# Kernel tuning notes

Measured on AMD Instinct MI355X. Metric: run time of the kernel, lower is better.

## Reference

```python
import jax, jax.numpy as jnp
import numpy as np

N = 100000
E = 1600000
IN_DIM, HID_DIM, OUT_DIM = 128, 64, 64


def setup_inputs() -> dict:
    key = jax.random.key(0)
    ks = jax.random.split(key, 8)
    x = jax.random.normal(ks[0], (N, IN_DIM), dtype=jnp.float32)
    src = jax.random.randint(ks[1], (E,), 0, N, dtype=jnp.int32)
    dst = jax.random.randint(ks[2], (E,), 0, N, dtype=jnp.int32)
    edge_index = jnp.stack([src, dst], axis=0)
    edge_weight = jax.random.uniform(ks[3], (E,), dtype=jnp.float32)
    # GCNConv params: lin weight [out, in] (no bias in lin), separate bias [out]
    W1 = jax.random.normal(ks[4], (HID_DIM, IN_DIM), dtype=jnp.float32) / np.sqrt(IN_DIM)
    b1 = jnp.zeros((HID_DIM,), dtype=jnp.float32)
    W2 = jax.random.normal(ks[5], (OUT_DIM, HID_DIM), dtype=jnp.float32) / np.sqrt(HID_DIM)
    b2 = jnp.zeros((OUT_DIM,), dtype=jnp.float32)
    return {"x": x, "edge_index": edge_index, "edge_weight": edge_weight,
            "W1": W1, "b1": b1, "W2": W2, "b2": b2}


def _gcn_conv(x, src, dst, ew, W, b, n_nodes):
    # PyG GCNConv: add self-loops (weight 1), symmetric normalization,
    # linear transform, scatter-add aggregation at dst, then bias.
    loop = jnp.arange(n_nodes, dtype=src.dtype)
    src_full = jnp.concatenate([src, loop])          # [E+N]
    dst_full = jnp.concatenate([dst, loop])          # [E+N]
    ew_full = jnp.concatenate([ew, jnp.ones((n_nodes,), x.dtype)])
    deg = jax.ops.segment_sum(ew_full, dst_full, num_segments=n_nodes)
    dinv = jnp.where(deg > 0, jax.lax.rsqrt(deg), 0.0)  # deg^{-1/2}, inf -> 0
    norm = dinv[src_full] * ew_full * dinv[dst_full]    # [E+N]
    h = x @ W.T                                          # [N, out]
    msgs = h[src_full] * norm[:, None]                   # gather + scale
    out = jax.ops.segment_sum(msgs, dst_full, num_segments=n_nodes)
    return out + b


def reference(x, edge_index, edge_weight, W1, b1, W2, b2):
    src, dst = edge_index[0], edge_index[1]
    h = _gcn_conv(x, src, dst, edge_weight, W1, b1, N)
    h = jax.nn.relu(h)
    # dropout is identity in eval mode (training=False)
    out = _gcn_conv(h, src, dst, edge_weight, W2, b2, N)
    return out
```

## Files before the change

kernel.cpp:

```cpp
#include <hip/hip_runtime.h>
#include <hip/hip_fp16.h>


constexpr float FXS     = 1048576.0f;
constexpr float FXS_INV = 1.0f / 1048576.0f;
constexpr int   SH      = 8;
constexpr int   CAP     = 5120;
constexpr int   NBMAX   = 512;
constexpr int   PW      = 256;
constexpr int   RPW     = 264;
constexpr int   BINA_BLOCKS = 256;

__device__ void binA_body(int bid, int nblocks,
                          const int* __restrict__ src, const int* __restrict__ dst,
                          const float* __restrict__ ew,
                          int* __restrict__ bktcur, int2* __restrict__ stage,
                          int E, int N) {
    __shared__ int cnt[NBMAX], gbase[NBMAX];
    const int tid = threadIdx.x;
    const int tot = E + N;
    const int nchunks = (tot + 2047) >> 11;
    for (int c = bid; c < nchunks; c += nblocks) {
        const int base = c << 11;
        for (int i = tid; i < NBMAX; i += 256) cnt[i] = 0;
        __syncthreads();
        int bkt[8], rank[8], pck[8];
        float w[8];
        #pragma unroll
        for (int j = 0; j < 8; ++j) {
            int e = base + j * 256 + tid;
            bkt[j] = -1;
            if (e < tot) {
                int s, t; float wv;
                if (e < E) { t = dst[e]; s = src[e]; wv = ew[e]; }
                else       { t = e - E;  s = t;      wv = 1.0f; }
                bkt[j] = t >> SH;
                pck[j] = ((t & 255) << 17) | s;
                w[j] = wv;
                rank[j] = atomicAdd(&cnt[bkt[j]], 1);
            }
        }
        __syncthreads();
        for (int i = tid; i < NBMAX; i += 256)
            if (cnt[i] > 0) gbase[i] = atomicAdd(&bktcur[i], cnt[i]);
        __syncthreads();
        #pragma unroll
        for (int j = 0; j < 8; ++j)
            if (bkt[j] >= 0) {
                int p = gbase[bkt[j]] + rank[j];
                if (p < CAP)
                    stage[(size_t)bkt[j] * CAP + p] =
                        make_int2(pck[j], __float_as_int(w[j]));
            }
        __syncthreads();
    }
}

template <int K, bool RELU>
__device__ void gemm_body(int bid, const float* __restrict__ X,
                          const float* __restrict__ W,
                          __half* __restrict__ H, int n) {
    constexpr int BK = 64, BK4 = 16;
    constexpr int XP = 68, WP = 68;
    __shared__ float Xs[64 * XP];
    __shared__ float Ws[BK * WP];
    const int tid = threadIdx.x;
    const int bn0 = bid * 64;
    const int tx = tid & 15, ty = tid >> 4;
    const int f0 = 4 * tx, nl = 4 * ty;

    float acc[4][4] = {};

    for (int kb = 0; kb < K; kb += BK) {
        #pragma unroll
        for (int it = 0; it < 4; ++it) {
            int idx = tid + it * 256;
            int node = idx >> 4, k4 = idx & 15;
            int g = bn0 + node;
            float4 v = make_float4(0.f, 0.f, 0.f, 0.f);
            if (g < n)
                v = *reinterpret_cast<const float4*>(X + (size_t)g * K + kb + 4 * k4);
            if (RELU) {
                v.x = fmaxf(v.x, 0.f); v.y = fmaxf(v.y, 0.f);
                v.z = fmaxf(v.z, 0.f); v.w = fmaxf(v.w, 0.f);
            }
            *reinterpret_cast<float4*>(&Xs[node * XP + 4 * k4]) = v;
        }
        #pragma unroll
        for (int it = 0; it < 4; ++it) {
            int idx = tid + it * 256;
            int feat = idx >> 4, k4 = idx & 15;
            float4 v = *reinterpret_cast<const float4*>(W + feat * K + kb + 4 * k4);
            Ws[(4 * k4 + 0) * WP + feat] = v.x;
            Ws[(4 * k4 + 1) * WP + feat] = v.y;
            Ws[(4 * k4 + 2) * WP + feat] = v.z;
            Ws[(4 * k4 + 3) * WP + feat] = v.w;
        }
        __syncthreads();

        #pragma unroll 4
        for (int k4 = 0; k4 < BK4; ++k4) {
            float4 xv[4], wv[4];
            #pragma unroll
            for (int i = 0; i < 4; ++i)
                xv[i] = *reinterpret_cast<const float4*>(&Xs[(nl + i) * XP + 4 * k4]);
            #pragma unroll
            for (int c = 0; c < 4; ++c)
                wv[c] = *reinterpret_cast<const float4*>(&Ws[(4 * k4 + c) * WP + f0]);
            #pragma unroll
            for (int i = 0; i < 4; ++i) {
                const float xc[4] = {xv[i].x, xv[i].y, xv[i].z, xv[i].w};
                #pragma unroll
                for (int c = 0; c < 4; ++c) {
                    acc[i][0] = fmaf(xc[c], wv[c].x, acc[i][0]);
                    acc[i][1] = fmaf(xc[c], wv[c].y, acc[i][1]);
                    acc[i][2] = fmaf(xc[c], wv[c].z, acc[i][2]);
                    acc[i][3] = fmaf(xc[c], wv[c].w, acc[i][3]);
                }
            }
        }
        __syncthreads();
    }

    #pragma unroll
    for (int i = 0; i < 4; ++i) {
        int g = bn0 + nl + i;
        if (g < n) {
            union { __half h[4]; uint2 u; } cv;
            cv.h[0] = __float2half_rn(acc[i][0]);
            cv.h[1] = __float2half_rn(acc[i][1]);
            cv.h[2] = __float2half_rn(acc[i][2]);
            cv.h[3] = __float2half_rn(acc[i][3]);
            *reinterpret_cast<uint2*>(H + ((size_t)g << 6) + f0) = cv.u;
        }
    }
}

__global__ __launch_bounds__(256, 4) void k_fat(const int* __restrict__ ei,
                                                const float* __restrict__ ew,
                                                int* __restrict__ bktcur,
                                                int2* __restrict__ stage,
                                                const float* __restrict__ x,
                                                const float* __restrict__ W1,
                                                __half* __restrict__ h16,
                                                int E, int N) {
    if (blockIdx.x < BINA_BLOCKS)
        binA_body(blockIdx.x, BINA_BLOCKS, ei, ei + E, ew, bktcur, stage, E, N);
    else
        gemm_body<128, false>(blockIdx.x - BINA_BLOCKS, x, W1, h16, N);
}

__global__ __launch_bounds__(256, 4) void k_gemm2(const float* __restrict__ X,
                                                  const float* __restrict__ W,
                                                  __half* __restrict__ H, int n) {
    gemm_body<64, true>(blockIdx.x, X, W, H, n);
}

__global__ __launch_bounds__(256) void k_histsort(
    const int2* __restrict__ stage, const int* __restrict__ bsizes,
    float* __restrict__ dinv, int* __restrict__ rowptr,
    int* __restrict__ winstart, int2* __restrict__ edata,
    const float* __restrict__ b1, const float* __restrict__ b2,
    float* __restrict__ agg1, float* __restrict__ dout,
    int N, int NB, int Etot) {
    __shared__ int2 eb[CAP];
    __shared__ unsigned long long hh[256];
    __shared__ int psum[256];
    __shared__ int cur[256];
    __shared__ float df[256];
    const int tid = threadIdx.x, b = blockIdx.x;

    int part = 0;
    for (int i = tid; i < b; i += 256) part += min(bsizes[i], CAP);
    psum[tid] = part;
    __syncthreads();
    for (int off = 128; off > 0; off >>= 1) {
        if (tid < off) psum[tid] += psum[tid + off];
        __syncthreads();
    }
    const int base = psum[0];
    const int len = min(bsizes[b], CAP);
    __syncthreads();

    hh[tid] = 0ull;
    __syncthreads();
    for (int i = tid; i < len; i += 256) {
        int2 en = stage[(size_t)b * CAP + i];
        eb[i] = en;
        unsigned long long fx = __float2uint_rn(__int_as_float(en.y) * FXS);
        atomicAdd(&hh[((unsigned)en.x) >> 17], (1ull << 32) | fx);
    }
    __syncthreads();

    const int c = (int)(hh[tid] >> 32);
    psum[tid] = c;
    __syncthreads();
    for (int off = 1; off < 256; off <<= 1) {
        int xv = (tid >= off) ? psum[tid - off] : 0;
        __syncthreads();
        psum[tid] += xv;
        __syncthreads();
    }
    const int rs = base + psum[tid] - c;
    const int g = (b << SH) + tid;
    float dv = 0.f;
    if (g < N) {
        dv = rsqrtf((float)(hh[tid] & 0xffffffffull) * FXS_INV);
        dinv[g] = dv;
        rowptr[g] = rs;
        const int re = rs + c;
        for (int w = (rs + PW - 1) / PW; w * PW < re; ++w) winstart[w] = g;
        if ((rs / PW) != ((re - 1) / PW)) {
            const float4* pb1 = (const float4*)b1;
            const float4* pb2 = (const float4*)b2;
            float4* pa = (float4*)(agg1 + ((size_t)g << 6));
            float4* po = (float4*)(dout + ((size_t)g << 6));
            #pragma unroll
            for (int j = 0; j < 16; ++j) { pa[j] = pb1[j]; po[j] = pb2[j]; }
        }
    }
    cur[tid] = rs;
    df[tid] = dv;
    if (b == 0 && tid == 0) rowptr[N] = Etot;
    __syncthreads();

    for (int i = tid; i < len; i += 256) {
        int2 en = eb[i];
        int local = ((unsigned)en.x) >> 17;
        int s = en.x & 0x1FFFF;
        float wsc = __int_as_float(en.y) * df[local];
        int pos = atomicAdd(&cur[local], 1);
        edata[pos] = make_int2(s, __float_as_int(wsc));
    }
}

__global__ __launch_bounds__(256) void k_pull(const int* __restrict__ rowptr,
                                              const int* __restrict__ winstart,
                                              const int2* __restrict__ edata,
                                              const __half* __restrict__ H,
                                              const float* __restrict__ dinv,
                                              const float* __restrict__ bias,
                                              float* __restrict__ AGG,
                                              int nW, int Etot, int N) {
    __shared__ int2 eb[4][PW];
    __shared__ int rp[4][RPW];
    const int wv = threadIdx.x >> 6, lane = threadIdx.x & 63;
    const int gq = lane >> 4;
    const int f4 = (lane & 15) * 4;
    const float4 bs = *reinterpret_cast<const float4*>(bias + f4);
    const int wid = blockIdx.x * 4 + wv;
    if (wid >= nW) return;
    const int e0 = wid * PW;
    const int e1 = min(e0 + PW, Etot);
    #pragma unroll
    for (int j = 0; j < PW / 64; ++j) {
        int e = e0 + j * 64 + lane;
        if (e < Etot) eb[wv][j * 64 + lane] = edata[e];
    }
    const int n0 = winstart[wid];
    #pragma unroll
    for (int j = 0; j < (RPW + 63) / 64; ++j) {
        int idx = j * 64 + lane;
        if (idx < RPW) {
            int nn = n0 + idx;
            rp[wv][idx] = (nn <= N) ? rowptr[nn] : Etot;
        }
    }
    int n = n0, e = e0;
    int rs = rp[wv][0];
    while (e < e1) {
        const int ni = n - n0 + 1;
        const int re = (ni < RPW) ? rp[wv][ni] : rowptr[n + 1];
        const int seg_end = min(re, e1);
        if (seg_end > e) {
            float a0 = 0.f, a1 = 0.f, a2 = 0.f, a3 = 0.f;
            int i = e - e0;
            const int iend = seg_end - e0;
            for (; i + 16 <= iend; i += 16) {
                int2 ed[4];
                uint2 hv[4];
                float ds[4];
                #pragma unroll
                for (int j = 0; j < 4; ++j) ed[j] = eb[wv][i + 4 * j + gq];
                #pragma unroll
                for (int j = 0; j < 4; ++j)
                    hv[j] = *reinterpret_cast<const uint2*>(
                        H + (((size_t)ed[j].x) << 6) + f4);
                #pragma unroll
                for (int j = 0; j < 4; ++j) ds[j] = dinv[ed[j].x];
                #pragma unroll
                for (int j = 0; j < 4; ++j) {
                    const float nr = ds[j] * __int_as_float(ed[j].y);
                    const __half2* ph = reinterpret_cast<const __half2*>(&hv[j]);
                    float2 p01 = __half22float2(ph[0]);
                    float2 p23 = __half22float2(ph[1]);
                    a0 = fmaf(p01.x, nr, a0);
                    a1 = fmaf(p01.y, nr, a1);
                    a2 = fmaf(p23.x, nr, a2);
                    a3 = fmaf(p23.y, nr, a3);
                }
            }
            for (; i < iend; i += 4) {
                int idx = i + gq;
                int2 ed = eb[wv][min(idx, iend - 1)];
                float nr = (idx < iend)
                               ? dinv[ed.x] * __int_as_float(ed.y) : 0.f;
                uint2 hv = *reinterpret_cast<const uint2*>(
                    H + (((size_t)ed.x) << 6) + f4);
                const __half2* ph = reinterpret_cast<const __half2*>(&hv);
                float2 p01 = __half22float2(ph[0]);
                float2 p23 = __half22float2(ph[1]);
                a0 = fmaf(p01.x, nr, a0);
                a1 = fmaf(p01.y, nr, a1);
                a2 = fmaf(p23.x, nr, a2);
                a3 = fmaf(p23.y, nr, a3);
            }
            a0 += __shfl_xor(a0, 16); a0 += __shfl_xor(a0, 32);
            a1 += __shfl_xor(a1, 16); a1 += __shfl_xor(a1, 32);
            a2 += __shfl_xor(a2, 16); a2 += __shfl_xor(a2, 32);
            a3 += __shfl_xor(a3, 16); a3 += __shfl_xor(a3, 32);
            if (lane < 16) {
                float* p = AGG + ((size_t)n << 6) + f4;
                if (rs >= e0 && re <= e1) {
                    *reinterpret_cast<float4*>(p) =
                        make_float4(a0 + bs.x, a1 + bs.y, a2 + bs.z, a3 + bs.w);
                } else {
                    atomicAdd(p + 0, a0);
                    atomicAdd(p + 1, a1);
                    atomicAdd(p + 2, a2);
                    atomicAdd(p + 3, a3);
                }
            }
        }
        e = seg_end;
        rs = re;
        ++n;
    }
}

extern "C" void kernel_launch(void* const* d_in, const int* in_sizes, int n_in,
                              void* d_out, int out_size, void* d_ws, size_t ws_size,
                              hipStream_t stream) {
    const float* x  = (const float*)d_in[0];
    const int*   ei = (const int*)d_in[1];
    const float* ew = (const float*)d_in[2];
    const float* W1 = (const float*)d_in[3];
    const float* b1 = (const float*)d_in[4];
    const float* W2 = (const float*)d_in[5];
    const float* b2 = (const float*)d_in[6];

    const int N = in_sizes[0] / 128;
    const int E = in_sizes[2];
    const int Etot = E + N;
    const int NB = (N + 255) >> SH;
    const int nW = (Etot + PW - 1) / PW;

    float* ws = (float*)d_ws;
    size_t o = 0;
    float*  dinv     = ws + o;            o += N;
    int*    rowptr   = (int*)(ws + o);    o += (size_t)N + 1;
    int*    winstart = (int*)(ws + o);    o += nW;
    int*    bktcur   = (int*)(ws + o);    o += NBMAX;
    o = (o + 1) & ~(size_t)1;
    int2*   edata    = (int2*)(ws + o);   o += 2 * (size_t)Etot;
    int2*   stage    = (int2*)(ws + o);   o += 2 * (size_t)NB * CAP;
    __half* h16      = (__half*)(ws + o); o += 32 * (size_t)N;
    float*  agg1     = ws + o;            o += 64 * (size_t)N;
    float*  out      = (float*)d_out;

    dim3 blk(256);
    const int gemm_blocks = (N + 63) / 64;

    hipMemsetAsync(bktcur, 0, NBMAX * sizeof(int), stream);
    k_fat<<<BINA_BLOCKS + gemm_blocks, blk, 0, stream>>>(ei, ew, bktcur, stage,
                                                         x, W1, h16, E, N);
    k_histsort<<<NB, blk, 0, stream>>>(stage, bktcur, dinv, rowptr, winstart,
                                       edata, b1, b2, agg1, out, N, NB, Etot);

    const int pull_blocks = (nW + 3) / 4;
    k_pull<<<pull_blocks, blk, 0, stream>>>(rowptr, winstart, edata, h16, dinv,
                                            b1, agg1, nW, Etot, N);
    k_gemm2<<<gemm_blocks, blk, 0, stream>>>(agg1, W2, h16, N);
    k_pull<<<pull_blocks, blk, 0, stream>>>(rowptr, winstart, edata, h16, dinv,
                                            b2, out, nW, Etot, N);
}
```

Before: 235.4 us.

## Split feature matrix into 16-column quarter planes and pull per quarter

```diff
diff --git a/kernel.cpp b/kernel.cpp
--- a/kernel.cpp
+++ b/kernel.cpp
@@ -59,7 +59,7 @@
 template <int K, bool RELU>
 __device__ void gemm_body(int bid, const float* __restrict__ X,
                           const float* __restrict__ W,
-                          __half* __restrict__ H, int n) {
+                          __half* __restrict__ Hq, int n) {
     constexpr int BK = 64, BK4 = 16;
     constexpr int XP = 68, WP = 68;
     __shared__ float Xs[64 * XP];
@@ -122,6 +122,7 @@
         __syncthreads();
     }
 
+    const int q = f0 >> 4, r = f0 & 15;
     #pragma unroll
     for (int i = 0; i < 4; ++i) {
         int g = bn0 + nl + i;
@@ -131,7 +132,7 @@
             cv.h[1] = __float2half_rn(acc[i][1]);
             cv.h[2] = __float2half_rn(acc[i][2]);
             cv.h[3] = __float2half_rn(acc[i][3]);
-            *reinterpret_cast<uint2*>(H + ((size_t)g << 6) + f0) = cv.u;
+            *reinterpret_cast<uint2*>(Hq + ((size_t)q * n + g) * 16 + r) = cv.u;
         }
     }
 }
@@ -142,32 +143,29 @@
                                                 int2* __restrict__ stage,
                                                 const float* __restrict__ x,
                                                 const float* __restrict__ W1,
-                                                __half* __restrict__ h16,
+                                                __half* __restrict__ Hq,
                                                 int E, int N) {
     if (blockIdx.x < BINA_BLOCKS)
         binA_body(blockIdx.x, BINA_BLOCKS, ei, ei + E, ew, bktcur, stage, E, N);
     else
-        gemm_body<128, false>(blockIdx.x - BINA_BLOCKS, x, W1, h16, N);
+        gemm_body<128, false>(blockIdx.x - BINA_BLOCKS, x, W1, Hq, N);
 }
 
 __global__ __launch_bounds__(256, 4) void k_gemm2(const float* __restrict__ X,
                                                   const float* __restrict__ W,
-                                                  __half* __restrict__ H, int n) {
-    gemm_body<64, true>(blockIdx.x, X, W, H, n);
-}
-
-__global__ __launch_bounds__(256) void k_histsort(
+                                                  __half* __restrict__ Hq, int n) {
+    gemm_body<64, true>(blockIdx.x, X, W, Hq, n);
+}
+
+__global__ __launch_bounds__(256) void k_hist(
     const int2* __restrict__ stage, const int* __restrict__ bsizes,
     float* __restrict__ dinv, int* __restrict__ rowptr,
-    int* __restrict__ winstart, int2* __restrict__ edata,
+    int* __restrict__ winstart,
     const float* __restrict__ b1, const float* __restrict__ b2,
     float* __restrict__ agg1, float* __restrict__ dout,
-    int N, int NB, int Etot) {
-    __shared__ int2 eb[CAP];
+    int N, int Etot) {
     __shared__ unsigned long long hh[256];
     __shared__ int psum[256];
-    __shared__ int cur[256];
-    __shared__ float df[256];
     const int tid = threadIdx.x, b = blockIdx.x;
 
     int part = 0;
@@ -186,7 +184,6 @@
     __syncthreads();
     for (int i = tid; i < len; i += 256) {
         int2 en = stage[(size_t)b * CAP + i];
-        eb[i] = en;
         unsigned long long fx = __float2uint_rn(__int_as_float(en.y) * FXS);
         atomicAdd(&hh[((unsigned)en.x) >> 17], (1ull << 32) | fx);
     }
@@ -203,10 +200,8 @@
     }
     const int rs = base + psum[tid] - c;
     const int g = (b << SH) + tid;
-    float dv = 0.f;
     if (g < N) {
-        dv = rsqrtf((float)(hh[tid] & 0xffffffffull) * FXS_INV);
-        dinv[g] = dv;
+        dinv[g] = rsqrtf((float)(hh[tid] & 0xffffffffull) * FXS_INV);
         rowptr[g] = rs;
         const int re = rs + c;
         for (int w = (rs + PW - 1) / PW; w * PW < re; ++w) winstart[w] = g;
@@ -219,37 +214,51 @@
             for (int j = 0; j < 16; ++j) { pa[j] = pb1[j]; po[j] = pb2[j]; }
         }
     }
-    cur[tid] = rs;
-    df[tid] = dv;
     if (b == 0 && tid == 0) rowptr[N] = Etot;
-    __syncthreads();
-
+}
+
+__global__ __launch_bounds__(256) void k_sort(const int2* __restrict__ stage,
+                                              const int* __restrict__ bsizes,
+                                              const int* __restrict__ rowptr,
+                                              const float* __restrict__ dinv,
+                                              int2* __restrict__ edata, int N) {
+    __shared__ int cur[256];
+    __shared__ float df[256];
+    const int tid = threadIdx.x, b = blockIdx.x;
+    const int g = (b << SH) + tid;
+    if (g < N) {
+        cur[tid] = rowptr[g];
+        df[tid] = dinv[g];
+    }
+    __syncthreads();
+    const int len = min(bsizes[b], CAP);
     for (int i = tid; i < len; i += 256) {
-        int2 en = eb[i];
+        int2 en = stage[(size_t)b * CAP + i];
         int local = ((unsigned)en.x) >> 17;
         int s = en.x & 0x1FFFF;
-        float wsc = __int_as_float(en.y) * df[local];
+        float nr = dinv[s] * __int_as_float(en.y) * df[local];
         int pos = atomicAdd(&cur[local], 1);
-        edata[pos] = make_int2(s, __float_as_int(wsc));
-    }
-}
-
-__global__ __launch_bounds__(256) void k_pull(const int* __restrict__ rowptr,
-                                              const int* __restrict__ winstart,
-                                              const int2* __restrict__ edata,
-                                              const __half* __restrict__ H,
-                                              const float* __restrict__ dinv,
-                                              const float* __restrict__ bias,
-                                              float* __restrict__ AGG,
-                                              int nW, int Etot, int N) {
+        edata[pos] = make_int2(s, __float_as_int(nr));
+    }
+}
+
+__global__ __launch_bounds__(256) void k_pullq(const int* __restrict__ rowptr,
+                                               const int* __restrict__ winstart,
+                                               const int2* __restrict__ edata,
+                                               const __half* __restrict__ Hq,
+                                               const float* __restrict__ bias,
+                                               float* __restrict__ AGG,
+                                               int nW, int Etot, int N, int BPP) {
     __shared__ int2 eb[4][PW];
     __shared__ int rp[4][RPW];
     const int wv = threadIdx.x >> 6, lane = threadIdx.x & 63;
     const int gq = lane >> 4;
-    const int f4 = (lane & 15) * 4;
-    const float4 bs = *reinterpret_cast<const float4*>(bias + f4);
-    const int wid = blockIdx.x * 4 + wv;
+    const int f  = lane & 15;
+    const int qPass = blockIdx.x / BPP;
+    const int wid = (blockIdx.x - qPass * BPP) * 4 + wv;
     if (wid >= nW) return;
+    const __half* HB = Hq + (size_t)qPass * N * 16;
+    const float bf = bias[(qPass << 4) + f];
     const int e0 = wid * PW;
     const int e1 = min(e0 + PW, Etot);
     #pragma unroll
@@ -273,63 +282,33 @@
         const int re = (ni < RPW) ? rp[wv][ni] : rowptr[n + 1];
         const int seg_end = min(re, e1);
         if (seg_end > e) {
-            float a0 = 0.f, a1 = 0.f, a2 = 0.f, a3 = 0.f;
+            float a = 0.f;
             int i = e - e0;
             const int iend = seg_end - e0;
             for (; i + 16 <= iend; i += 16) {
                 int2 ed[4];
-                uint2 hv[4];
-                float ds[4];
+                __half hv[4];
                 #pragma unroll
                 for (int j = 0; j < 4; ++j) ed[j] = eb[wv][i + 4 * j + gq];
                 #pragma unroll
                 for (int j = 0; j < 4; ++j)
-                    hv[j] = *reinterpret_cast<const uint2*>(
-                        H + (((size_t)ed[j].x) << 6) + f4);
+                    hv[j] = HB[(size_t)ed[j].x * 16 + f];
                 #pragma unroll
-                for (int j = 0; j < 4; ++j) ds[j] = dinv[ed[j].x];
-                #pragma unroll
-                for (int j = 0; j < 4; ++j) {
-                    const float nr = ds[j] * __int_as_float(ed[j].y);
-                    const __half2* ph = reinterpret_cast<const __half2*>(&hv[j]);
-                    float2 p01 = __half22float2(ph[0]);
-                    float2 p23 = __half22float2(ph[1]);
-                    a0 = fmaf(p01.x, nr, a0);
-                    a1 = fmaf(p01.y, nr, a1);
-                    a2 = fmaf(p23.x, nr, a2);
-                    a3 = fmaf(p23.y, nr, a3);
-                }
+                for (int j = 0; j < 4; ++j)
+                    a = fmaf(__half2float(hv[j]), __int_as_float(ed[j].y), a);
             }
             for (; i < iend; i += 4) {
                 int idx = i + gq;
                 int2 ed = eb[wv][min(idx, iend - 1)];
-                float nr = (idx < iend)
-                               ? dinv[ed.x] * __int_as_float(ed.y) : 0.f;
-                uint2 hv = *reinterpret_cast<const uint2*>(
-                    H + (((size_t)ed.x) << 6) + f4);
-                const __half2* ph = reinterpret_cast<const __half2*>(&hv);
-                float2 p01 = __half22float2(ph[0]);
-                float2 p23 = __half22float2(ph[1]);
-                a0 = fmaf(p01.x, nr, a0);
-                a1 = fmaf(p01.y, nr, a1);
-                a2 = fmaf(p23.x, nr, a2);
-                a3 = fmaf(p23.y, nr, a3);
-            }
-            a0 += __shfl_xor(a0, 16); a0 += __shfl_xor(a0, 32);
-            a1 += __shfl_xor(a1, 16); a1 += __shfl_xor(a1, 32);
-            a2 += __shfl_xor(a2, 16); a2 += __shfl_xor(a2, 32);
-            a3 += __shfl_xor(a3, 16); a3 += __shfl_xor(a3, 32);
+                float nr = (idx < iend) ? __int_as_float(ed.y) : 0.f;
+                a = fmaf(__half2float(HB[(size_t)ed.x * 16 + f]), nr, a);
+            }
+            a += __shfl_xor(a, 16);
+            a += __shfl_xor(a, 32);
             if (lane < 16) {
-                float* p = AGG + ((size_t)n << 6) + f4;
-                if (rs >= e0 && re <= e1) {
-                    *reinterpret_cast<float4*>(p) =
-                        make_float4(a0 + bs.x, a1 + bs.y, a2 + bs.z, a3 + bs.w);
-                } else {
-                    atomicAdd(p + 0, a0);
-                    atomicAdd(p + 1, a1);
-                    atomicAdd(p + 2, a2);
-                    atomicAdd(p + 3, a3);
-                }
+                float* p = AGG + ((size_t)n << 6) + (qPass << 4) + lane;
+                if (rs >= e0 && re <= e1) *p = a + bf;
+                else atomicAdd(p, a);
             }
         }
         e = seg_end;
@@ -354,6 +333,7 @@
     const int Etot = E + N;
     const int NB = (N + 255) >> SH;
     const int nW = (Etot + PW - 1) / PW;
+    const int BPP = (nW + 3) / 4;
 
     float* ws = (float*)d_ws;
     size_t o = 0;
@@ -364,7 +344,7 @@
     o = (o + 1) & ~(size_t)1;
     int2*   edata    = (int2*)(ws + o);   o += 2 * (size_t)Etot;
     int2*   stage    = (int2*)(ws + o);   o += 2 * (size_t)NB * CAP;
-    __half* h16      = (__half*)(ws + o); o += 32 * (size_t)N;
+    __half* Hq       = (__half*)(ws + o); o += 32 * (size_t)N;
     float*  agg1     = ws + o;            o += 64 * (size_t)N;
     float*  out      = (float*)d_out;
 
@@ -373,14 +353,14 @@
 
     hipMemsetAsync(bktcur, 0, NBMAX * sizeof(int), stream);
     k_fat<<<BINA_BLOCKS + gemm_blocks, blk, 0, stream>>>(ei, ew, bktcur, stage,
-                                                         x, W1, h16, E, N);
-    k_histsort<<<NB, blk, 0, stream>>>(stage, bktcur, dinv, rowptr, winstart,
-                                       edata, b1, b2, agg1, out, N, NB, Etot);
-
-    const int pull_blocks = (nW + 3) / 4;
-    k_pull<<<pull_blocks, blk, 0, stream>>>(rowptr, winstart, edata, h16, dinv,
-                                            b1, agg1, nW, Etot, N);
-    k_gemm2<<<gemm_blocks, blk, 0, stream>>>(agg1, W2, h16, N);
-    k_pull<<<pull_blocks, blk, 0, stream>>>(rowptr, winstart, edata, h16, dinv,
-                                            b2, out, nW, Etot, N);
-}
+                                                         x, W1, Hq, E, N);
+    k_hist<<<NB, blk, 0, stream>>>(stage, bktcur, dinv, rowptr, winstart,
+                                   b1, b2, agg1, out, N, Etot);
+    k_sort<<<NB, blk, 0, stream>>>(stage, bktcur, rowptr, dinv, edata, N);
+
+    k_pullq<<<4 * BPP, blk, 0, stream>>>(rowptr, winstart, edata, Hq, b1, agg1,
+                                         nW, Etot, N, BPP);
+    k_gemm2<<<gemm_blocks, blk, 0, stream>>>(agg1, W2, Hq, N);
+    k_pullq<<<4 * BPP, blk, 0, stream>>>(rowptr, winstart, edata, Hq, b2, out,
+                                         nW, Etot, N, BPP);
+}
```

Measured after the change: 326.7 us. +38.8%, slower.

## Handle self-loops analytically and fold full edge normalization into sorted edge data

Applied to the files above, without the earlier changes.

```diff
diff --git a/kernel.cpp b/kernel.cpp
--- a/kernel.cpp
+++ b/kernel.cpp
@@ -15,11 +15,10 @@
                           const int* __restrict__ src, const int* __restrict__ dst,
                           const float* __restrict__ ew,
                           int* __restrict__ bktcur, int2* __restrict__ stage,
-                          int E, int N) {
+                          int E) {
     __shared__ int cnt[NBMAX], gbase[NBMAX];
     const int tid = threadIdx.x;
-    const int tot = E + N;
-    const int nchunks = (tot + 2047) >> 11;
+    const int nchunks = (E + 2047) >> 11;
     for (int c = bid; c < nchunks; c += nblocks) {
         const int base = c << 11;
         for (int i = tid; i < NBMAX; i += 256) cnt[i] = 0;
@@ -30,13 +29,11 @@
         for (int j = 0; j < 8; ++j) {
             int e = base + j * 256 + tid;
             bkt[j] = -1;
-            if (e < tot) {
-                int s, t; float wv;
-                if (e < E) { t = dst[e]; s = src[e]; wv = ew[e]; }
-                else       { t = e - E;  s = t;      wv = 1.0f; }
+            if (e < E) {
+                int t = dst[e];
                 bkt[j] = t >> SH;
-                pck[j] = ((t & 255) << 17) | s;
-                w[j] = wv;
+                pck[j] = ((t & 255) << 17) | src[e];
+                w[j] = ew[e];
                 rank[j] = atomicAdd(&cnt[bkt[j]], 1);
             }
         }
@@ -56,10 +53,14 @@
     }
 }
 
-template <int K, bool RELU>
+template <int K, bool RELU, bool BINIT>
 __device__ void gemm_body(int bid, const float* __restrict__ X,
                           const float* __restrict__ W,
-                          __half* __restrict__ H, int n) {
+                          __half* __restrict__ H, int n,
+                          const char* __restrict__ flags,
+                          const float* __restrict__ dinv,
+                          const float* __restrict__ bias,
+                          float* __restrict__ OUT) {
     constexpr int BK = 64, BK4 = 16;
     constexpr int XP = 68, WP = 68;
     __shared__ float Xs[64 * XP];
@@ -132,6 +133,18 @@
             cv.h[2] = __float2half_rn(acc[i][2]);
             cv.h[3] = __float2half_rn(acc[i][3]);
             *reinterpret_cast<uint2*>(H + ((size_t)g << 6) + f0) = cv.u;
+            if (BINIT) {
+                if (flags[g]) {
+                    const float d = dinv[g];
+                    const float d2 = d * d;
+                    const float4 bs = *reinterpret_cast<const float4*>(bias + f0);
+                    *reinterpret_cast<float4*>(OUT + ((size_t)g << 6) + f0) =
+                        make_float4(fmaf(acc[i][0], d2, bs.x),
+                                    fmaf(acc[i][1], d2, bs.y),
+                                    fmaf(acc[i][2], d2, bs.z),
+                                    fmaf(acc[i][3], d2, bs.w));
+                }
+            }
         }
     }
 }
@@ -145,29 +158,30 @@
                                                 __half* __restrict__ h16,
                                                 int E, int N) {
     if (blockIdx.x < BINA_BLOCKS)
-        binA_body(blockIdx.x, BINA_BLOCKS, ei, ei + E, ew, bktcur, stage, E, N);
+        binA_body(blockIdx.x, BINA_BLOCKS, ei, ei + E, ew, bktcur, stage, E);
     else
-        gemm_body<128, false>(blockIdx.x - BINA_BLOCKS, x, W1, h16, N);
+        gemm_body<128, false, false>(blockIdx.x - BINA_BLOCKS, x, W1, h16, N,
+                                     nullptr, nullptr, nullptr, nullptr);
 }
 
 __global__ __launch_bounds__(256, 4) void k_gemm2(const float* __restrict__ X,
                                                   const float* __restrict__ W,
-                                                  __half* __restrict__ H, int n) {
-    gemm_body<64, true>(blockIdx.x, X, W, H, n);
-}
-
-__global__ __launch_bounds__(256) void k_histsort(
+                                                  __half* __restrict__ H, int n,
+                                                  const char* __restrict__ flags,
+                                                  const float* __restrict__ dinv,
+                                                  const float* __restrict__ bias,
+                                                  float* __restrict__ OUT) {
+    gemm_body<64, true, true>(blockIdx.x, X, W, H, n, flags, dinv, bias, OUT);
+}
+
+__global__ __launch_bounds__(256) void k_hist(
     const int2* __restrict__ stage, const int* __restrict__ bsizes,
     float* __restrict__ dinv, int* __restrict__ rowptr,
-    int* __restrict__ winstart, int2* __restrict__ edata,
-    const float* __restrict__ b1, const float* __restrict__ b2,
-    float* __restrict__ agg1, float* __restrict__ dout,
-    int N, int NB, int Etot) {
-    __shared__ int2 eb[CAP];
+    int* __restrict__ winstart, char* __restrict__ flags,
+    const __half* __restrict__ h16, const float* __restrict__ b1,
+    float* __restrict__ agg1, int N, int E) {
     __shared__ unsigned long long hh[256];
     __shared__ int psum[256];
-    __shared__ int cur[256];
-    __shared__ float df[256];
     const int tid = threadIdx.x, b = blockIdx.x;
 
     int part = 0;
@@ -186,7 +200,6 @@
     __syncthreads();
     for (int i = tid; i < len; i += 256) {
         int2 en = stage[(size_t)b * CAP + i];
-        eb[i] = en;
         unsigned long long fx = __float2uint_rn(__int_as_float(en.y) * FXS);
         atomicAdd(&hh[((unsigned)en.x) >> 17], (1ull << 32) | fx);
     }
@@ -203,34 +216,55 @@
     }
     const int rs = base + psum[tid] - c;
     const int g = (b << SH) + tid;
-    float dv = 0.f;
     if (g < N) {
-        dv = rsqrtf((float)(hh[tid] & 0xffffffffull) * FXS_INV);
+        const float dv =
+            rsqrtf(1.0f + (float)(hh[tid] & 0xffffffffull) * FXS_INV);
         dinv[g] = dv;
         rowptr[g] = rs;
         const int re = rs + c;
         for (int w = (rs + PW - 1) / PW; w * PW < re; ++w) winstart[w] = g;
-        if ((rs / PW) != ((re - 1) / PW)) {
-            const float4* pb1 = (const float4*)b1;
-            const float4* pb2 = (const float4*)b2;
+        const bool flagged = (c == 0) || ((rs / PW) != ((re - 1) / PW));
+        flags[g] = flagged ? 1 : 0;
+        if (flagged) {
+            const float d2 = dv * dv;
+            const __half2* hp = (const __half2*)(h16 + ((size_t)g << 6));
+            const float4* pb = (const float4*)b1;
             float4* pa = (float4*)(agg1 + ((size_t)g << 6));
-            float4* po = (float4*)(dout + ((size_t)g << 6));
             #pragma unroll
-            for (int j = 0; j < 16; ++j) { pa[j] = pb1[j]; po[j] = pb2[j]; }
-        }
-    }
-    cur[tid] = rs;
-    df[tid] = dv;
-    if (b == 0 && tid == 0) rowptr[N] = Etot;
-    __syncthreads();
-
+            for (int j = 0; j < 16; ++j) {
+                float2 fA = __half22float2(hp[2 * j]);
+                float2 fB = __half22float2(hp[2 * j + 1]);
+                float4 bb = pb[j];
+                pa[j] = make_float4(fmaf(fA.x, d2, bb.x), fmaf(fA.y, d2, bb.y),
+                                    fmaf(fB.x, d2, bb.z), fmaf(fB.y, d2, bb.w));
+            }
+        }
+    }
+    if (b == 0 && tid == 0) rowptr[N] = E;
+}
+
+__global__ __launch_bounds__(256) void k_sort(const int2* __restrict__ stage,
+                                              const int* __restrict__ bsizes,
+                                              const int* __restrict__ rowptr,
+                                              const float* __restrict__ dinv,
+                                              int2* __restrict__ edata, int N) {
+    __shared__ int cur[256];
+    __shared__ float df[256];
+    const int tid = threadIdx.x, b = blockIdx.x;
+    const int g = (b << SH) + tid;
+    if (g < N) {
+        cur[tid] = rowptr[g];
+        df[tid] = dinv[g];
+    }
+    __syncthreads();
+    const int len = min(bsizes[b], CAP);
     for (int i = tid; i < len; i += 256) {
-        int2 en = eb[i];
+        int2 en = stage[(size_t)b * CAP + i];
         int local = ((unsigned)en.x) >> 17;
         int s = en.x & 0x1FFFF;
-        float wsc = __int_as_float(en.y) * df[local];
+        float nr = dinv[s] * __int_as_float(en.y) * df[local];
         int pos = atomicAdd(&cur[local], 1);
-        edata[pos] = make_int2(s, __float_as_int(wsc));
+        edata[pos] = make_int2(s, __float_as_int(nr));
     }
 }
 
@@ -241,7 +275,7 @@
                                               const float* __restrict__ dinv,
                                               const float* __restrict__ bias,
                                               float* __restrict__ AGG,
-                                              int nW, int Etot, int N) {
+                                              int nW, int E, int N) {
     __shared__ int2 eb[4][PW];
     __shared__ int rp[4][RPW];
     const int wv = threadIdx.x >> 6, lane = threadIdx.x & 63;
@@ -251,11 +285,11 @@
     const int wid = blockIdx.x * 4 + wv;
     if (wid >= nW) return;
     const int e0 = wid * PW;
-    const int e1 = min(e0 + PW, Etot);
+    const int e1 = min(e0 + PW, E);
     #pragma unroll
     for (int j = 0; j < PW / 64; ++j) {
         int e = e0 + j * 64 + lane;
-        if (e < Etot) eb[wv][j * 64 + lane] = edata[e];
+        if (e < E) eb[wv][j * 64 + lane] = edata[e];
     }
     const int n0 = winstart[wid];
     #pragma unroll
@@ -263,23 +297,24 @@
         int idx = j * 64 + lane;
         if (idx < RPW) {
             int nn = n0 + idx;
-            rp[wv][idx] = (nn <= N) ? rowptr[nn] : Etot;
+            rp[wv][idx] = (nn <= N) ? rowptr[nn] : E;
         }
     }
     int n = n0, e = e0;
     int rs = rp[wv][0];
     while (e < e1) {
-        const int ni = n - n0 + 1;
-        const int re = (ni < RPW) ? rp[wv][ni] : rowptr[n + 1];
+        const int re = rp[wv][n - n0 + 1];
         const int seg_end = min(re, e1);
         if (seg_end > e) {
+            const uint2 hs = *reinterpret_cast<const uint2*>(
+                H + ((size_t)n << 6) + f4);
+            const float dv = dinv[n];
             float a0 = 0.f, a1 = 0.f, a2 = 0.f, a3 = 0.f;
             int i = e - e0;
             const int iend = seg_end - e0;
             for (; i + 16 <= iend; i += 16) {
                 int2 ed[4];
                 uint2 hv[4];
-                float ds[4];
                 #pragma unroll
                 for (int j = 0; j < 4; ++j) ed[j] = eb[wv][i + 4 * j + gq];
                 #pragma unroll
@@ -287,10 +322,8 @@
                     hv[j] = *reinterpret_cast<const uint2*>(
                         H + (((size_t)ed[j].x) << 6) + f4);
                 #pragma unroll
-                for (int j = 0; j < 4; ++j) ds[j] = dinv[ed[j].x];
-                #pragma unroll
                 for (int j = 0; j < 4; ++j) {
-                    const float nr = ds[j] * __int_as_float(ed[j].y);
+                    const float nr = __int_as_float(ed[j].y);
                     const __half2* ph = reinterpret_cast<const __half2*>(&hv[j]);
                     float2 p01 = __half22float2(ph[0]);
                     float2 p23 = __half22float2(ph[1]);
@@ -303,8 +336,7 @@
             for (; i < iend; i += 4) {
                 int idx = i + gq;
                 int2 ed = eb[wv][min(idx, iend - 1)];
-                float nr = (idx < iend)
-                               ? dinv[ed.x] * __int_as_float(ed.y) : 0.f;
+                float nr = (idx < iend) ? __int_as_float(ed.y) : 0.f;
                 uint2 hv = *reinterpret_cast<const uint2*>(
                     H + (((size_t)ed.x) << 6) + f4);
                 const __half2* ph = reinterpret_cast<const __half2*>(&hv);
@@ -322,8 +354,13 @@
             if (lane < 16) {
                 float* p = AGG + ((size_t)n << 6) + f4;
                 if (rs >= e0 && re <= e1) {
-                    *reinterpret_cast<float4*>(p) =
-                        make_float4(a0 + bs.x, a1 + bs.y, a2 + bs.z, a3 + bs.w);
+                    const float d2 = dv * dv;
+                    const __half2* ph = reinterpret_cast<const __half2*>(&hs);
+                    float2 s01 = __half22float2(ph[0]);
+                    float2 s23 = __half22float2(ph[1]);
+                    *reinterpret_cast<float4*>(p) = make_float4(
+                        fmaf(s01.x, d2, bs.x) + a0, fmaf(s01.y, d2, bs.y) + a1,
+                        fmaf(s23.x, d2, bs.z) + a2, fmaf(s23.y, d2, bs.w) + a3);
                 } else {
                     atomicAdd(p + 0, a0);
                     atomicAdd(p + 1, a1);
@@ -351,9 +388,8 @@
 
     const int N = in_sizes[0] / 128;
     const int E = in_sizes[2];
-    const int Etot = E + N;
     const int NB = (N + 255) >> SH;
-    const int nW = (Etot + PW - 1) / PW;
+    const int nW = (E + PW - 1) / PW;
 
     float* ws = (float*)d_ws;
     size_t o = 0;
@@ -361,8 +397,9 @@
     int*    rowptr   = (int*)(ws + o);    o += (size_t)N + 1;
     int*    winstart = (int*)(ws + o);    o += nW;
     int*    bktcur   = (int*)(ws + o);    o += NBMAX;
+    char*   flags    = (char*)(ws + o);   o += (N + 3) / 4;
     o = (o + 1) & ~(size_t)1;
-    int2*   edata    = (int2*)(ws + o);   o += 2 * (size_t)Etot;
+    int2*   edata    = (int2*)(ws + o);   o += 2 * (size_t)E;
     int2*   stage    = (int2*)(ws + o);   o += 2 * (size_t)NB * CAP;
     __half* h16      = (__half*)(ws + o); o += 32 * (size_t)N;
     float*  agg1     = ws + o;            o += 64 * (size_t)N;
@@ -374,13 +411,15 @@
     hipMemsetAsync(bktcur, 0, NBMAX * sizeof(int), stream);
     k_fat<<<BINA_BLOCKS + gemm_blocks, blk, 0, stream>>>(ei, ew, bktcur, stage,
                                                          x, W1, h16, E, N);
-    k_histsort<<<NB, blk, 0, stream>>>(stage, bktcur, dinv, rowptr, winstart,
-                                       edata, b1, b2, agg1, out, N, NB, Etot);
+    k_hist<<<NB, blk, 0, stream>>>(stage, bktcur, dinv, rowptr, winstart,
+                                   flags, h16, b1, agg1, N, E);
+    k_sort<<<NB, blk, 0, stream>>>(stage, bktcur, rowptr, dinv, edata, N);
 
     const int pull_blocks = (nW + 3) / 4;
     k_pull<<<pull_blocks, blk, 0, stream>>>(rowptr, winstart, edata, h16, dinv,
-                                            b1, agg1, nW, Etot, N);
-    k_gemm2<<<gemm_blocks, blk, 0, stream>>>(agg1, W2, h16, N);
+                                            b1, agg1, nW, E, N);
+    k_gemm2<<<gemm_blocks, blk, 0, stream>>>(agg1, W2, h16, N, flags, dinv,
+                                             b2, out);
     k_pull<<<pull_blocks, blk, 0, stream>>>(rowptr, winstart, edata, h16, dinv,
-                                            b2, out, nW, Etot, N);
-}
+                                            b2, out, nW, E, N);
+}
```

After: 226.3 us. 3.8% less time.
